# Performance work log

Hardware: AMD Instinct MI355X
Metric: run time of the kernel (lower is better)

Reference implementation:

```python
import jax, jax.numpy as jnp
import numpy as np

L = 8        # len_prog
E = 8        # experts per layer (uniform dsl_num)
D = 256      # embed_dim
B = 16384    # batch_size
H1, H2 = 64, 32  # MyMLP hidden dims


def setup_inputs() -> dict:
    key = jax.random.key(0)
    ks = jax.random.split(key, 8)
    s1 = 1.0 / np.sqrt(D)
    s2 = 1.0 / np.sqrt(H1)
    s3 = 1.0 / np.sqrt(H2)
    return {
        "src_embeddings": jax.random.normal(ks[0], (B, D), jnp.float32),
        "W1": jax.random.normal(ks[1], (L, E, H1, D), jnp.float32) * s1,
        "b1": jax.random.normal(ks[2], (L, E, H1), jnp.float32) * s1,
        "W2": jax.random.normal(ks[3], (L, E, H2, H1), jnp.float32) * s2,
        "b2": jax.random.normal(ks[4], (L, E, H2), jnp.float32) * s2,
        "W3": jax.random.normal(ks[5], (L, E, D, H2), jnp.float32) * s3,
        "b3": jax.random.normal(ks[6], (L, E, D), jnp.float32) * s3,
        "masks": jax.random.normal(ks[7], (L, B, E), jnp.float32) * 0.1,
    }


def reference(src_embeddings, W1, b1, W2, b2, W3, b3, masks):
    # Per layer: run E small expert MLPs on the same x, then combine with
    # softmax(mask) over the expert axis (torch path: masks=None -> softmax).
    def layer(x, params):
        w1, bb1, w2, bb2, w3, bb3, m = params
        h = jax.nn.relu(jnp.einsum('bd,ehd->beh', x, w1) + bb1)      # [B,E,H1]
        h = jax.nn.relu(jnp.einsum('beh,ekh->bek', h, w2) + bb2)     # [B,E,H2]
        out = jnp.einsum('bek,edk->bed', h, w3) + bb3                # [B,E,D]
        w = jax.nn.softmax(m, axis=-1)                               # [B,E]
        x_new = jnp.einsum('be,bed->bd', w, out)                     # [B,D]
        return x_new, None

    x, _ = jax.lax.scan(layer, src_embeddings, (W1, b1, W2, b2, W3, b3, masks))
    return x
```

## Files before the change

kernel.cpp:

```cpp
#include <hip/hip_runtime.h>
#include <hip/hip_bf16.h>

#define LNUM 8
#define ENUM 8
#define DDIM 256
#define BSZ  16384
#define H1N  64
#define H2N  32

#define BT   32
#define NTHR 256

#define PX   264
#define PH1  72
#define PH2  40
#define PSW  9

#define WS1_OFF 0
#define WS2_OFF 1048576
#define WS3_OFF 1179648

typedef float f32x4 __attribute__((ext_vector_type(4)));
typedef unsigned short u16x8 __attribute__((ext_vector_type(8)));
typedef unsigned short u16x4 __attribute__((ext_vector_type(4)));
typedef __bf16 bf16x8 __attribute__((ext_vector_type(8)));

#define Z4 ((f32x4){0.f, 0.f, 0.f, 0.f})

static __device__ __forceinline__ unsigned short f2bf(float f) {
    __bf16 h = (__bf16)f;
    return __builtin_bit_cast(unsigned short, h);
}

static __device__ __forceinline__ f32x4 mfma16(u16x8 a, u16x8 b, f32x4 c) {
    return __builtin_amdgcn_mfma_f32_16x16x32_bf16(
        __builtin_bit_cast(bf16x8, a), __builtin_bit_cast(bf16x8, b), c, 0, 0, 0);
}

static __device__ __forceinline__ void lbar() {
    asm volatile("s_waitcnt lgkmcnt(0)" ::: "memory");
    __builtin_amdgcn_s_barrier();
    asm volatile("" ::: "memory");
}

__global__ __launch_bounds__(256) void cvt_w_frag(
    const float* __restrict__ w1, const float* __restrict__ w2,
    const float* __restrict__ w3, unsigned short* __restrict__ ws)
{
    int gid = blockIdx.x * 256 + threadIdx.x;
    const float* src;
    unsigned short* dst;
    if (gid < 131072) {
        int s = gid >> 11, rem = gid & 2047;
        int n = rem >> 5, kc = rem & 31;
        int nt = n >> 4, r = n & 15, kt = kc >> 2, q = kc & 3;
        src = w1 + (size_t)gid * 8;
        dst = ws + WS1_OFF + (size_t)s * 16384 + nt * 4096 + kt * 512 + (q * 16 + r) * 8;
    } else if (gid < 147456) {
        int g = gid - 131072;
        int s = g >> 8, rem = g & 255;
        int n = rem >> 3, kc = rem & 7;
        int n2 = n >> 4, r = n & 15, kt = kc >> 2, q = kc & 3;
        src = w2 + (size_t)g * 8;
        dst = ws + WS2_OFF + (size_t)s * 2048 + n2 * 1024 + kt * 512 + (q * 16 + r) * 8;
    } else {
        int g = gid - 147456;
        int s = g >> 10, rem = g & 1023;
        int n = rem >> 2, q = rem & 3;
        int nt = n >> 4, r = n & 15;
        src = w3 + (size_t)g * 8;
        dst = ws + WS3_OFF + (size_t)s * 8192 + nt * 512 + (q * 16 + r) * 8;
    }
    float4 a = *(const float4*)src;
    float4 b = *(const float4*)(src + 4);
    u16x8 p;
    p[0] = f2bf(a.x); p[1] = f2bf(a.y); p[2] = f2bf(a.z); p[3] = f2bf(a.w);
    p[4] = f2bf(b.x); p[5] = f2bf(b.y); p[6] = f2bf(b.z); p[7] = f2bf(b.w);
    *(u16x8*)dst = p;
}

__global__ __launch_bounds__(NTHR, 2) void moe_fused(
    const float* __restrict__ src, const unsigned short* __restrict__ Wf,
    const float* __restrict__ b1, const float* __restrict__ b2,
    const float* __restrict__ b3, const float* __restrict__ masks,
    float* __restrict__ out)
{
    __shared__ __align__(16) unsigned short Xlds[BT * PX];
    __shared__ __align__(16) unsigned short H1T[2][BT * PH1];
    __shared__ __align__(16) unsigned short H2T[2][BT * PH2];
    __shared__ float SWlds[BT * PSW];

    const int tid  = threadIdx.x;
    const int lane = tid & 63;
    const int wn   = tid >> 6;
    const int rg   = wn & 1;
    const int fg   = wn >> 1;
    const int n15  = lane & 15;
    const int q    = lane >> 4;
    const int b0   = blockIdx.x * BT;

    const unsigned short* w1base = Wf + WS1_OFF + wn * 4096 + lane * 8;
    const unsigned short* w2base = Wf + WS2_OFF + fg * 1024 + lane * 8;
    const unsigned short* w3base = Wf + WS3_OFF + wn * 2048 + lane * 8;

    u16x8 xf[2][8];
    f32x4 ACC[2][4];

    auto stage_softmax = [&](int l) {
        if (tid < BT) {
            const float* mp = masks + ((size_t)l * BSZ + b0 + tid) * ENUM;
            float4 m0 = *(const float4*)mp;
            float4 m1 = *(const float4*)(mp + 4);
            float mv[8] = {m0.x, m0.y, m0.z, m0.w, m1.x, m1.y, m1.z, m1.w};
            float mx = mv[0];
            #pragma unroll
            for (int e = 1; e < 8; ++e) mx = fmaxf(mx, mv[e]);
            float s = 0.f;
            #pragma unroll
            for (int e = 0; e < 8; ++e) { mv[e] = expf(mv[e] - mx); s += mv[e]; }
            float inv = 1.f / s;
            #pragma unroll
            for (int e = 0; e < 8; ++e) SWlds[tid * PSW + e] = mv[e] * inv;
        }
    };

    auto acc_init = [&](int l) {
        const float* b3l = b3 + (size_t)l * ENUM * DDIM;
        #pragma unroll
        for (int mt = 0; mt < 2; ++mt)
            #pragma unroll
            for (int nt = 0; nt < 4; ++nt) ACC[mt][nt] = Z4;
        #pragma unroll 2
        for (int e2 = 0; e2 < ENUM; ++e2) {
            float swv[2][4];
            #pragma unroll
            for (int mt = 0; mt < 2; ++mt)
                #pragma unroll
                for (int rr = 0; rr < 4; ++rr)
                    swv[mt][rr] = SWlds[(mt*16 + q*4 + rr) * PSW + e2];
            #pragma unroll
            for (int nt = 0; nt < 4; ++nt) {
                float bv = b3l[e2 * DDIM + wn*64 + nt*16 + n15];
                #pragma unroll
                for (int mt = 0; mt < 2; ++mt)
                    #pragma unroll
                    for (int rr = 0; rr < 4; ++rr)
                        ACC[mt][nt][rr] += swv[mt][rr] * bv;
            }
        }
    };

    auto xf_read = [&]() {
        #pragma unroll
        for (int mt = 0; mt < 2; ++mt)
            #pragma unroll
            for (int kt = 0; kt < 8; ++kt)
                xf[mt][kt] = *(const u16x8*)
                    &Xlds[(mt*16 + n15) * PX + q*8 + kt*32];
    };
    auto x_write = [&]() {
        #pragma unroll
        for (int mt = 0; mt < 2; ++mt)
            #pragma unroll
            for (int nt = 0; nt < 4; ++nt)
                #pragma unroll
                for (int rr = 0; rr < 4; ++rr)
                    Xlds[(mt*16 + q*4 + rr) * PX + wn*64 + nt*16 + n15] =
                        f2bf(ACC[mt][nt][rr]);
    };

    #pragma unroll
    for (int i = 0; i < 4; ++i) {
        int o = (i * NTHR + tid) * 8;
        int r = o >> 8, c = o & 255;
        const float* p = src + (size_t)(b0 + r) * DDIM + c;
        float4 f0 = *(const float4*)(p);
        float4 f1 = *(const float4*)(p + 4);
        u16x8 pk;
        pk[0] = f2bf(f0.x); pk[1] = f2bf(f0.y); pk[2] = f2bf(f0.z); pk[3] = f2bf(f0.w);
        pk[4] = f2bf(f1.x); pk[5] = f2bf(f1.y); pk[6] = f2bf(f1.z); pk[7] = f2bf(f1.w);
        *(u16x8*)&Xlds[r * PX + c] = pk;
    }
    stage_softmax(0);
    __syncthreads();
    xf_read();
    acc_init(0);

    #pragma unroll 1
    for (int ss = 0; ss < LNUM * ENUM / 2; ++ss) {
        const int s0 = 2 * ss, s1 = s0 + 1;
        const int l  = s0 >> 3, e0 = s0 & 7, e1 = s1 & 7;

        u16x8 wfA[8], wfB[8], w2A[2], w2B[2];
        {
            const unsigned short* pA = w1base + (size_t)s0 * 16384;
            const unsigned short* pB = w1base + (size_t)s1 * 16384;
            #pragma unroll
            for (int kt = 0; kt < 8; ++kt) {
                wfA[kt] = *(const u16x8*)(pA + kt * 512);
                wfB[kt] = *(const u16x8*)(pB + kt * 512);
            }
            const unsigned short* q2A = w2base + (size_t)s0 * 2048;
            const unsigned short* q2B = w2base + (size_t)s1 * 2048;
            w2A[0] = *(const u16x8*)(q2A);  w2A[1] = *(const u16x8*)(q2A + 512);
            w2B[0] = *(const u16x8*)(q2B);  w2B[1] = *(const u16x8*)(q2B + 512);
        }
        const float4 bb1A = *(const float4*)(b1 + s0 * 64 + wn * 16 + q * 4);
        const float4 bb1B = *(const float4*)(b1 + s1 * 64 + wn * 16 + q * 4);
        const float4 bb2A = *(const float4*)(b2 + s0 * 32 + fg * 16 + q * 4);
        const float4 bb2B = *(const float4*)(b2 + s1 * 32 + fg * 16 + q * 4);

        f32x4 a1A[2] = {Z4, Z4}, a1B[2] = {Z4, Z4};
        #pragma unroll
        for (int kt = 0; kt < 8; ++kt) {
            a1A[0] = mfma16(wfA[kt], xf[0][kt], a1A[0]);
            a1A[1] = mfma16(wfA[kt], xf[1][kt], a1A[1]);
            a1B[0] = mfma16(wfB[kt], xf[0][kt], a1B[0]);
            a1B[1] = mfma16(wfB[kt], xf[1][kt], a1B[1]);
        }

        u16x8 w3A[4], w3B[4];
        {
            const unsigned short* p3A = w3base + (size_t)s0 * 8192;
            const unsigned short* p3B = w3base + (size_t)s1 * 8192;
            #pragma unroll
            for (int nt = 0; nt < 4; ++nt) {
                w3A[nt] = *(const u16x8*)(p3A + nt * 512);
                w3B[nt] = *(const u16x8*)(p3B + nt * 512);
            }
        }

        #pragma unroll
        for (int mt = 0; mt < 2; ++mt) {
            u16x4 pkA, pkB;
            #pragma unroll
            for (int rr = 0; rr < 4; ++rr) {
                pkA[rr] = f2bf(fmaxf(a1A[mt][rr] + bb1A[rr], 0.f));
                pkB[rr] = f2bf(fmaxf(a1B[mt][rr] + bb1B[rr], 0.f));
            }
            int row = mt*16 + n15;
            *(u16x4*)&H1T[0][row * PH1 + wn*16 + q*4] = pkA;
            *(u16x4*)&H1T[1][row * PH1 + wn*16 + q*4] = pkB;
        }
        lbar();

        f32x4 a2A = Z4, a2B = Z4;
        {
            int hrow = rg*16 + n15;
            u16x8 hA0 = *(const u16x8*)&H1T[0][hrow * PH1 + q*8];
            u16x8 hA1 = *(const u16x8*)&H1T[0][hrow * PH1 + q*8 + 32];
            u16x8 hB0 = *(const u16x8*)&H1T[1][hrow * PH1 + q*8];
            u16x8 hB1 = *(const u16x8*)&H1T[1][hrow * PH1 + q*8 + 32];
            a2A = mfma16(w2A[0], hA0, a2A);
            a2B = mfma16(w2B[0], hB0, a2B);
            a2A = mfma16(w2A[1], hA1, a2A);
            a2B = mfma16(w2B[1], hB1, a2B);
        }
        {
            int row = rg*16 + n15;
            float swA = SWlds[row * PSW + e0];
            float swB = SWlds[row * PSW + e1];
            u16x4 pkA, pkB;
            #pragma unroll
            for (int rr = 0; rr < 4; ++rr) {
                pkA[rr] = f2bf(fmaxf(a2A[rr] + bb2A[rr], 0.f) * swA);
                pkB[rr] = f2bf(fmaxf(a2B[rr] + bb2B[rr], 0.f) * swB);
            }
            *(u16x4*)&H2T[0][row * PH2 + fg*16 + q*4] = pkA;
            *(u16x4*)&H2T[1][row * PH2 + fg*16 + q*4] = pkB;
        }
        lbar();

        {
            u16x8 hA0 = *(const u16x8*)&H2T[0][(n15) * PH2 + q*8];
            u16x8 hA1 = *(const u16x8*)&H2T[0][(16 + n15) * PH2 + q*8];
            u16x8 hB0 = *(const u16x8*)&H2T[1][(n15) * PH2 + q*8];
            u16x8 hB1 = *(const u16x8*)&H2T[1][(16 + n15) * PH2 + q*8];
            #pragma unroll
            for (int nt = 0; nt < 4; ++nt) {
                ACC[0][nt] = mfma16(hA0, w3A[nt], ACC[0][nt]);
                ACC[1][nt] = mfma16(hA1, w3A[nt], ACC[1][nt]);
            }
            #pragma unroll
            for (int nt = 0; nt < 4; ++nt) {
                ACC[0][nt] = mfma16(hB0, w3B[nt], ACC[0][nt]);
                ACC[1][nt] = mfma16(hB1, w3B[nt], ACC[1][nt]);
            }
        }

        if (e1 == 7 && l < LNUM - 1) {
            x_write();
            lbar();
            xf_read();
            stage_softmax(l + 1);
            lbar();
            acc_init(l + 1);
        }
    }

    #pragma unroll
    for (int mt = 0; mt < 2; ++mt)
        #pragma unroll
        for (int nt = 0; nt < 4; ++nt)
            #pragma unroll
            for (int rr = 0; rr < 4; ++rr)
                out[(size_t)(b0 + mt*16 + q*4 + rr) * DDIM
                    + wn*64 + nt*16 + n15] = ACC[mt][nt][rr];
}

extern "C" void kernel_launch(void* const* d_in, const int* in_sizes, int n_in,
                              void* d_out, int out_size, void* d_ws, size_t ws_size,
                              hipStream_t stream) {
    const float* src   = (const float*)d_in[0];
    const float* W1    = (const float*)d_in[1];
    const float* b1    = (const float*)d_in[2];
    const float* W2    = (const float*)d_in[3];
    const float* b2    = (const float*)d_in[4];
    const float* W3    = (const float*)d_in[5];
    const float* b3    = (const float*)d_in[6];
    const float* masks = (const float*)d_in[7];
    float* out = (float*)d_out;
    unsigned short* ws = (unsigned short*)d_ws;

    hipLaunchKernelGGL(cvt_w_frag, dim3(832), dim3(256), 0, stream, W1, W2, W3, ws);
    hipLaunchKernelGGL(moe_fused, dim3(BSZ / BT), dim3(NTHR), 0, stream,
                       src, ws, b1, b2, b3, masks, out);
}
```

Before: 178.1 us.

## Software-pipeline the three expert GEMM stages across expert pairs with double-buffered LDS

Restructures the per-layer loop so that G1 of the next expert pair, G2 of the current pair and G3 of the previous pair run in the same barrier interval. H1T and H2T get double buffers indexed by parity, which cuts the number of barriers per expert pair. It also raises launch bounds to 4 waves-per-EU occupancy and adds s_setprio around the MFMA bursts. The cost is higher register pressure under the tighter occupancy target, with possible spilling, plus more LDS per block.

```diff
diff --git a/kernel.cpp b/kernel.cpp
--- a/kernel.cpp
+++ b/kernel.cpp
@@ -79,15 +79,15 @@
     *(u16x8*)dst = p;
 }
 
-__global__ __launch_bounds__(NTHR, 2) void moe_fused(
+__global__ __launch_bounds__(NTHR, 4) void moe_fused(
     const float* __restrict__ src, const unsigned short* __restrict__ Wf,
     const float* __restrict__ b1, const float* __restrict__ b2,
     const float* __restrict__ b3, const float* __restrict__ masks,
     float* __restrict__ out)
 {
     __shared__ __align__(16) unsigned short Xlds[BT * PX];
-    __shared__ __align__(16) unsigned short H1T[2][BT * PH1];
-    __shared__ __align__(16) unsigned short H2T[2][BT * PH2];
+    __shared__ __align__(16) unsigned short H1T[2][2][BT * PH1];
+    __shared__ __align__(16) unsigned short H2T[2][2][BT * PH2];
     __shared__ float SWlds[BT * PSW];
 
     const int tid  = threadIdx.x;
@@ -167,6 +167,109 @@
                 for (int rr = 0; rr < 4; ++rr)
                     Xlds[(mt*16 + q*4 + rr) * PX + wn*64 + nt*16 + n15] =
                         f2bf(ACC[mt][nt][rr]);
+    };
+
+    auto load_W1p = [&](int P, u16x8* A, u16x8* B) {
+        const unsigned short* pA = w1base + (size_t)(2*P) * 16384;
+        const unsigned short* pB = pA + 16384;
+        #pragma unroll
+        for (int kt = 0; kt < 8; ++kt) {
+            A[kt] = *(const u16x8*)(pA + kt * 512);
+            B[kt] = *(const u16x8*)(pB + kt * 512);
+        }
+    };
+    auto load_W2p = [&](int P, u16x8* A, u16x8* B) {
+        const unsigned short* qA = w2base + (size_t)(2*P) * 2048;
+        const unsigned short* qB = qA + 2048;
+        A[0] = *(const u16x8*)(qA);  A[1] = *(const u16x8*)(qA + 512);
+        B[0] = *(const u16x8*)(qB);  B[1] = *(const u16x8*)(qB + 512);
+    };
+    auto load_W3p = [&](int P, u16x8* A, u16x8* B) {
+        const unsigned short* pA = w3base + (size_t)(2*P) * 8192;
+        const unsigned short* pB = pA + 8192;
+        #pragma unroll
+        for (int nt = 0; nt < 4; ++nt) {
+            A[nt] = *(const u16x8*)(pA + nt * 512);
+            B[nt] = *(const u16x8*)(pB + nt * 512);
+        }
+    };
+
+    auto do_G1 = [&](int par, const u16x8* wfA, const u16x8* wfB,
+                     float4 bb1A, float4 bb1B) {
+        f32x4 a1A[2] = {Z4, Z4}, a1B[2] = {Z4, Z4};
+        __builtin_amdgcn_s_setprio(1);
+        #pragma unroll
+        for (int kt = 0; kt < 8; ++kt) {
+            a1A[0] = mfma16(wfA[kt], xf[0][kt], a1A[0]);
+            a1A[1] = mfma16(wfA[kt], xf[1][kt], a1A[1]);
+            a1B[0] = mfma16(wfB[kt], xf[0][kt], a1B[0]);
+            a1B[1] = mfma16(wfB[kt], xf[1][kt], a1B[1]);
+        }
+        __builtin_amdgcn_s_setprio(0);
+        #pragma unroll
+        for (int mt = 0; mt < 2; ++mt) {
+            u16x4 pkA, pkB;
+            #pragma unroll
+            for (int rr = 0; rr < 4; ++rr) {
+                pkA[rr] = f2bf(fmaxf(a1A[mt][rr] + bb1A[rr], 0.f));
+                pkB[rr] = f2bf(fmaxf(a1B[mt][rr] + bb1B[rr], 0.f));
+            }
+            int row = mt*16 + n15;
+            *(u16x4*)&H1T[par][0][row * PH1 + wn*16 + q*4] = pkA;
+            *(u16x4*)&H1T[par][1][row * PH1 + wn*16 + q*4] = pkB;
+        }
+    };
+
+    auto do_G2 = [&](int e0, int par, const u16x8* w2A, const u16x8* w2B,
+                     float4 bb2A, float4 bb2B) {
+        f32x4 a2A = Z4, a2B = Z4;
+        int hrow = rg*16 + n15;
+        u16x8 hA0 = *(const u16x8*)&H1T[par][0][hrow * PH1 + q*8];
+        u16x8 hA1 = *(const u16x8*)&H1T[par][0][hrow * PH1 + q*8 + 32];
+        u16x8 hB0 = *(const u16x8*)&H1T[par][1][hrow * PH1 + q*8];
+        u16x8 hB1 = *(const u16x8*)&H1T[par][1][hrow * PH1 + q*8 + 32];
+        a2A = mfma16(w2A[0], hA0, a2A);
+        a2B = mfma16(w2B[0], hB0, a2B);
+        a2A = mfma16(w2A[1], hA1, a2A);
+        a2B = mfma16(w2B[1], hB1, a2B);
+        float swA = SWlds[hrow * PSW + e0];
+        float swB = SWlds[hrow * PSW + e0 + 1];
+        u16x4 pkA, pkB;
+        #pragma unroll
+        for (int rr = 0; rr < 4; ++rr) {
+            pkA[rr] = f2bf(fmaxf(a2A[rr] + bb2A[rr], 0.f) * swA);
+            pkB[rr] = f2bf(fmaxf(a2B[rr] + bb2B[rr], 0.f) * swB);
+        }
+        *(u16x4*)&H2T[par][0][hrow * PH2 + fg*16 + q*4] = pkA;
+        *(u16x4*)&H2T[par][1][hrow * PH2 + fg*16 + q*4] = pkB;
+    };
+
+    auto do_G3 = [&](int par, const u16x8* w3A, const u16x8* w3B) {
+        u16x8 hA0 = *(const u16x8*)&H2T[par][0][(n15) * PH2 + q*8];
+        u16x8 hA1 = *(const u16x8*)&H2T[par][0][(16 + n15) * PH2 + q*8];
+        u16x8 hB0 = *(const u16x8*)&H2T[par][1][(n15) * PH2 + q*8];
+        u16x8 hB1 = *(const u16x8*)&H2T[par][1][(16 + n15) * PH2 + q*8];
+        __builtin_amdgcn_s_setprio(1);
+        #pragma unroll
+        for (int nt = 0; nt < 4; ++nt) {
+            ACC[0][nt] = mfma16(hA0, w3A[nt], ACC[0][nt]);
+            ACC[1][nt] = mfma16(hA1, w3A[nt], ACC[1][nt]);
+        }
+        #pragma unroll
+        for (int nt = 0; nt < 4; ++nt) {
+            ACC[0][nt] = mfma16(hB0, w3B[nt], ACC[0][nt]);
+            ACC[1][nt] = mfma16(hB1, w3B[nt], ACC[1][nt]);
+        }
+        __builtin_amdgcn_s_setprio(0);
+    };
+
+    auto ld_bb1 = [&](int P, float4& A, float4& B) {
+        A = *(const float4*)(b1 + (2*P) * 64 + wn * 16 + q * 4);
+        B = *(const float4*)(b1 + (2*P + 1) * 64 + wn * 16 + q * 4);
+    };
+    auto ld_bb2 = [&](int P, float4& A, float4& B) {
+        A = *(const float4*)(b2 + (2*P) * 32 + fg * 16 + q * 4);
+        B = *(const float4*)(b2 + (2*P + 1) * 32 + fg * 16 + q * 4);
     };
 
     #pragma unroll
@@ -187,108 +290,62 @@
     acc_init(0);
 
     #pragma unroll 1
-    for (int ss = 0; ss < LNUM * ENUM / 2; ++ss) {
-        const int s0 = 2 * ss, s1 = s0 + 1;
-        const int l  = s0 >> 3, e0 = s0 & 7, e1 = s1 & 7;
-
-        u16x8 wfA[8], wfB[8], w2A[2], w2B[2];
-        {
-            const unsigned short* pA = w1base + (size_t)s0 * 16384;
-            const unsigned short* pB = w1base + (size_t)s1 * 16384;
-            #pragma unroll
-            for (int kt = 0; kt < 8; ++kt) {
-                wfA[kt] = *(const u16x8*)(pA + kt * 512);
-                wfB[kt] = *(const u16x8*)(pB + kt * 512);
-            }
-            const unsigned short* q2A = w2base + (size_t)s0 * 2048;
-            const unsigned short* q2B = w2base + (size_t)s1 * 2048;
-            w2A[0] = *(const u16x8*)(q2A);  w2A[1] = *(const u16x8*)(q2A + 512);
-            w2B[0] = *(const u16x8*)(q2B);  w2B[1] = *(const u16x8*)(q2B + 512);
-        }
-        const float4 bb1A = *(const float4*)(b1 + s0 * 64 + wn * 16 + q * 4);
-        const float4 bb1B = *(const float4*)(b1 + s1 * 64 + wn * 16 + q * 4);
-        const float4 bb2A = *(const float4*)(b2 + s0 * 32 + fg * 16 + q * 4);
-        const float4 bb2B = *(const float4*)(b2 + s1 * 32 + fg * 16 + q * 4);
-
-        f32x4 a1A[2] = {Z4, Z4}, a1B[2] = {Z4, Z4};
-        #pragma unroll
-        for (int kt = 0; kt < 8; ++kt) {
-            a1A[0] = mfma16(wfA[kt], xf[0][kt], a1A[0]);
-            a1A[1] = mfma16(wfA[kt], xf[1][kt], a1A[1]);
-            a1B[0] = mfma16(wfB[kt], xf[0][kt], a1B[0]);
-            a1B[1] = mfma16(wfB[kt], xf[1][kt], a1B[1]);
-        }
-
-        u16x8 w3A[4], w3B[4];
-        {
-            const unsigned short* p3A = w3base + (size_t)s0 * 8192;
-            const unsigned short* p3B = w3base + (size_t)s1 * 8192;
-            #pragma unroll
-            for (int nt = 0; nt < 4; ++nt) {
-                w3A[nt] = *(const u16x8*)(p3A + nt * 512);
-                w3B[nt] = *(const u16x8*)(p3B + nt * 512);
-            }
-        }
-
-        #pragma unroll
-        for (int mt = 0; mt < 2; ++mt) {
-            u16x4 pkA, pkB;
-            #pragma unroll
-            for (int rr = 0; rr < 4; ++rr) {
-                pkA[rr] = f2bf(fmaxf(a1A[mt][rr] + bb1A[rr], 0.f));
-                pkB[rr] = f2bf(fmaxf(a1B[mt][rr] + bb1B[rr], 0.f));
-            }
-            int row = mt*16 + n15;
-            *(u16x4*)&H1T[0][row * PH1 + wn*16 + q*4] = pkA;
-            *(u16x4*)&H1T[1][row * PH1 + wn*16 + q*4] = pkB;
-        }
-        lbar();
-
-        f32x4 a2A = Z4, a2B = Z4;
-        {
-            int hrow = rg*16 + n15;
-            u16x8 hA0 = *(const u16x8*)&H1T[0][hrow * PH1 + q*8];
-            u16x8 hA1 = *(const u16x8*)&H1T[0][hrow * PH1 + q*8 + 32];
-            u16x8 hB0 = *(const u16x8*)&H1T[1][hrow * PH1 + q*8];
-            u16x8 hB1 = *(const u16x8*)&H1T[1][hrow * PH1 + q*8 + 32];
-            a2A = mfma16(w2A[0], hA0, a2A);
-            a2B = mfma16(w2B[0], hB0, a2B);
-            a2A = mfma16(w2A[1], hA1, a2A);
-            a2B = mfma16(w2B[1], hB1, a2B);
-        }
-        {
-            int row = rg*16 + n15;
-            float swA = SWlds[row * PSW + e0];
-            float swB = SWlds[row * PSW + e1];
-            u16x4 pkA, pkB;
-            #pragma unroll
-            for (int rr = 0; rr < 4; ++rr) {
-                pkA[rr] = f2bf(fmaxf(a2A[rr] + bb2A[rr], 0.f) * swA);
-                pkB[rr] = f2bf(fmaxf(a2B[rr] + bb2B[rr], 0.f) * swB);
-            }
-            *(u16x4*)&H2T[0][row * PH2 + fg*16 + q*4] = pkA;
-            *(u16x4*)&H2T[1][row * PH2 + fg*16 + q*4] = pkB;
-        }
-        lbar();
-
-        {
-            u16x8 hA0 = *(const u16x8*)&H2T[0][(n15) * PH2 + q*8];
-            u16x8 hA1 = *(const u16x8*)&H2T[0][(16 + n15) * PH2 + q*8];
-            u16x8 hB0 = *(const u16x8*)&H2T[1][(n15) * PH2 + q*8];
-            u16x8 hB1 = *(const u16x8*)&H2T[1][(16 + n15) * PH2 + q*8];
-            #pragma unroll
-            for (int nt = 0; nt < 4; ++nt) {
-                ACC[0][nt] = mfma16(hA0, w3A[nt], ACC[0][nt]);
-                ACC[1][nt] = mfma16(hA1, w3A[nt], ACC[1][nt]);
-            }
-            #pragma unroll
-            for (int nt = 0; nt < 4; ++nt) {
-                ACC[0][nt] = mfma16(hB0, w3B[nt], ACC[0][nt]);
-                ACC[1][nt] = mfma16(hB1, w3B[nt], ACC[1][nt]);
-            }
-        }
-
-        if (e1 == 7 && l < LNUM - 1) {
+    for (int l = 0; l < LNUM; ++l) {
+        const int P0 = 4 * l;
+
+        {
+            u16x8 wfA[8], wfB[8]; float4 bb1A, bb1B;
+            load_W1p(P0, wfA, wfB); ld_bb1(P0, bb1A, bb1B);
+            do_G1(0, wfA, wfB, bb1A, bb1B);
+            lbar();
+        }
+        {
+            u16x8 w2A[2], w2B[2], wfA[8], wfB[8];
+            float4 bb2A, bb2B, bb1A, bb1B;
+            load_W2p(P0, w2A, w2B); load_W1p(P0 + 1, wfA, wfB);
+            ld_bb2(P0, bb2A, bb2B); ld_bb1(P0 + 1, bb1A, bb1B);
+            do_G2(0, 0, w2A, w2B, bb2A, bb2B);
+            do_G1(1, wfA, wfB, bb1A, bb1B);
+            lbar();
+        }
+        {
+            u16x8 w2A[2], w2B[2], w3A[4], w3B[4], wfA[8], wfB[8];
+            float4 bb2A, bb2B, bb1A, bb1B;
+            load_W2p(P0 + 1, w2A, w2B); load_W3p(P0, w3A, w3B);
+            load_W1p(P0 + 2, wfA, wfB);
+            ld_bb2(P0 + 1, bb2A, bb2B); ld_bb1(P0 + 2, bb1A, bb1B);
+            do_G2(2, 1, w2A, w2B, bb2A, bb2B);
+            do_G3(0, w3A, w3B);
+            do_G1(0, wfA, wfB, bb1A, bb1B);
+            lbar();
+        }
+        {
+            u16x8 w2A[2], w2B[2], w3A[4], w3B[4], wfA[8], wfB[8];
+            float4 bb2A, bb2B, bb1A, bb1B;
+            load_W2p(P0 + 2, w2A, w2B); load_W3p(P0 + 1, w3A, w3B);
+            load_W1p(P0 + 3, wfA, wfB);
+            ld_bb2(P0 + 2, bb2A, bb2B); ld_bb1(P0 + 3, bb1A, bb1B);
+            do_G2(4, 0, w2A, w2B, bb2A, bb2B);
+            do_G3(1, w3A, w3B);
+            do_G1(1, wfA, wfB, bb1A, bb1B);
+            lbar();
+        }
+        {
+            u16x8 w2A[2], w2B[2], w3A[4], w3B[4];
+            float4 bb2A, bb2B;
+            load_W2p(P0 + 3, w2A, w2B); load_W3p(P0 + 2, w3A, w3B);
+            ld_bb2(P0 + 3, bb2A, bb2B);
+            do_G2(6, 1, w2A, w2B, bb2A, bb2B);
+            do_G3(0, w3A, w3B);
+            lbar();
+        }
+        {
+            u16x8 w3A[4], w3B[4];
+            load_W3p(P0 + 3, w3A, w3B);
+            do_G3(1, w3A, w3B);
+        }
+
+        if (l < LNUM - 1) {
             x_write();
             lbar();
             xf_read();
```

Result: slower. 243.1 us (+36.5%).

## Assign whole experts per wave for stages 1-2 to cut block barriers

Applied to the files above, without the earlier changes.

Instead of all four waves cooperating on each expert pair, which needs two block barriers per pair, each wave now computes the full first and second MLP layers for two experts privately. It uses a per-wave H1 buffer and writes all eight H2 tiles to LDS. A single barrier per layer precedes the cooperative third-layer accumulation over all experts. This removes most barriers, but increases per-wave register pressure, LDS footprint, and the serial first-layer work per wave.

```diff
diff --git a/kernel.cpp b/kernel.cpp
--- a/kernel.cpp
+++ b/kernel.cpp
@@ -86,22 +86,18 @@
     float* __restrict__ out)
 {
     __shared__ __align__(16) unsigned short Xlds[BT * PX];
-    __shared__ __align__(16) unsigned short H1T[2][BT * PH1];
-    __shared__ __align__(16) unsigned short H2T[2][BT * PH2];
+    __shared__ __align__(16) unsigned short H1W[4][BT * PH1];
+    __shared__ __align__(16) unsigned short H2T[8][BT * PH2];
     __shared__ float SWlds[BT * PSW];
 
     const int tid  = threadIdx.x;
     const int lane = tid & 63;
-    const int wn   = tid >> 6;
-    const int rg   = wn & 1;
-    const int fg   = wn >> 1;
+    const int wv   = tid >> 6;
     const int n15  = lane & 15;
     const int q    = lane >> 4;
     const int b0   = blockIdx.x * BT;
 
-    const unsigned short* w1base = Wf + WS1_OFF + wn * 4096 + lane * 8;
-    const unsigned short* w2base = Wf + WS2_OFF + fg * 1024 + lane * 8;
-    const unsigned short* w3base = Wf + WS3_OFF + wn * 2048 + lane * 8;
+    const unsigned short* w3base = Wf + WS3_OFF + wv * 2048 + lane * 8;
 
     u16x8 xf[2][8];
     f32x4 ACC[2][4];
@@ -140,7 +136,7 @@
                     swv[mt][rr] = SWlds[(mt*16 + q*4 + rr) * PSW + e2];
             #pragma unroll
             for (int nt = 0; nt < 4; ++nt) {
-                float bv = b3l[e2 * DDIM + wn*64 + nt*16 + n15];
+                float bv = b3l[e2 * DDIM + wv*64 + nt*16 + n15];
                 #pragma unroll
                 for (int mt = 0; mt < 2; ++mt)
                     #pragma unroll
@@ -165,7 +161,7 @@
             for (int nt = 0; nt < 4; ++nt)
                 #pragma unroll
                 for (int rr = 0; rr < 4; ++rr)
-                    Xlds[(mt*16 + q*4 + rr) * PX + wn*64 + nt*16 + n15] =
+                    Xlds[(mt*16 + q*4 + rr) * PX + wv*64 + nt*16 + n15] =
                         f2bf(ACC[mt][nt][rr]);
     };
 
@@ -184,117 +180,111 @@
     stage_softmax(0);
     __syncthreads();
     xf_read();
-    acc_init(0);
 
     #pragma unroll 1
-    for (int ss = 0; ss < LNUM * ENUM / 2; ++ss) {
-        const int s0 = 2 * ss, s1 = s0 + 1;
-        const int l  = s0 >> 3, e0 = s0 & 7, e1 = s1 & 7;
-
-        u16x8 wfA[8], wfB[8], w2A[2], w2B[2];
-        {
-            const unsigned short* pA = w1base + (size_t)s0 * 16384;
-            const unsigned short* pB = w1base + (size_t)s1 * 16384;
-            #pragma unroll
-            for (int kt = 0; kt < 8; ++kt) {
-                wfA[kt] = *(const u16x8*)(pA + kt * 512);
-                wfB[kt] = *(const u16x8*)(pB + kt * 512);
+    for (int l = 0; l < LNUM; ++l) {
+        const int sbase = l * ENUM;
+
+        #pragma unroll
+        for (int pe = 0; pe < 2; ++pe) {
+            const int e = wv + pe * 4;
+            const int s = sbase + e;
+
+            #pragma unroll
+            for (int ft = 0; ft < 4; ++ft) {
+                u16x8 w1f[8];
+                const unsigned short* p1 =
+                    Wf + WS1_OFF + (size_t)s * 16384 + ft * 4096 + lane * 8;
+                #pragma unroll
+                for (int kt = 0; kt < 8; ++kt)
+                    w1f[kt] = *(const u16x8*)(p1 + kt * 512);
+                f32x4 a1[2] = {Z4, Z4};
+                #pragma unroll
+                for (int kt = 0; kt < 8; ++kt) {
+                    a1[0] = mfma16(w1f[kt], xf[0][kt], a1[0]);
+                    a1[1] = mfma16(w1f[kt], xf[1][kt], a1[1]);
+                }
+                const float4 bb1 = *(const float4*)(b1 + s * 64 + ft * 16 + q * 4);
+                #pragma unroll
+                for (int mt = 0; mt < 2; ++mt) {
+                    u16x4 pk;
+                    #pragma unroll
+                    for (int rr = 0; rr < 4; ++rr)
+                        pk[rr] = f2bf(fmaxf(a1[mt][rr] + bb1[rr], 0.f));
+                    *(u16x4*)&H1W[wv][(mt*16 + n15) * PH1 + ft*16 + q*4] = pk;
+                }
             }
-            const unsigned short* q2A = w2base + (size_t)s0 * 2048;
-            const unsigned short* q2B = w2base + (size_t)s1 * 2048;
-            w2A[0] = *(const u16x8*)(q2A);  w2A[1] = *(const u16x8*)(q2A + 512);
-            w2B[0] = *(const u16x8*)(q2B);  w2B[1] = *(const u16x8*)(q2B + 512);
-        }
-        const float4 bb1A = *(const float4*)(b1 + s0 * 64 + wn * 16 + q * 4);
-        const float4 bb1B = *(const float4*)(b1 + s1 * 64 + wn * 16 + q * 4);
-        const float4 bb2A = *(const float4*)(b2 + s0 * 32 + fg * 16 + q * 4);
-        const float4 bb2B = *(const float4*)(b2 + s1 * 32 + fg * 16 + q * 4);
-
-        f32x4 a1A[2] = {Z4, Z4}, a1B[2] = {Z4, Z4};
-        #pragma unroll
-        for (int kt = 0; kt < 8; ++kt) {
-            a1A[0] = mfma16(wfA[kt], xf[0][kt], a1A[0]);
-            a1A[1] = mfma16(wfA[kt], xf[1][kt], a1A[1]);
-            a1B[0] = mfma16(wfB[kt], xf[0][kt], a1B[0]);
-            a1B[1] = mfma16(wfB[kt], xf[1][kt], a1B[1]);
-        }
-
-        u16x8 w3A[4], w3B[4];
-        {
-            const unsigned short* p3A = w3base + (size_t)s0 * 8192;
-            const unsigned short* p3B = w3base + (size_t)s1 * 8192;
+
+            {
+                u16x8 w2f[2][2];
+                const unsigned short* p2 =
+                    Wf + WS2_OFF + (size_t)s * 2048 + lane * 8;
+                #pragma unroll
+                for (int f2 = 0; f2 < 2; ++f2)
+                    #pragma unroll
+                    for (int kt = 0; kt < 2; ++kt)
+                        w2f[f2][kt] = *(const u16x8*)(p2 + f2*1024 + kt*512);
+                u16x8 h1f[2][2];
+                #pragma unroll
+                for (int mt = 0; mt < 2; ++mt)
+                    #pragma unroll
+                    for (int kt = 0; kt < 2; ++kt)
+                        h1f[mt][kt] = *(const u16x8*)
+                            &H1W[wv][(mt*16 + n15) * PH1 + q*8 + kt*32];
+                f32x4 a2[2][2] = {{Z4, Z4}, {Z4, Z4}};
+                #pragma unroll
+                for (int f2 = 0; f2 < 2; ++f2)
+                    #pragma unroll
+                    for (int mt = 0; mt < 2; ++mt)
+                        #pragma unroll
+                        for (int kt = 0; kt < 2; ++kt)
+                            a2[f2][mt] = mfma16(w2f[f2][kt], h1f[mt][kt], a2[f2][mt]);
+                float swv[2];
+                #pragma unroll
+                for (int mt = 0; mt < 2; ++mt)
+                    swv[mt] = SWlds[(mt*16 + n15) * PSW + e];
+                #pragma unroll
+                for (int f2 = 0; f2 < 2; ++f2) {
+                    const float4 bb2 = *(const float4*)(b2 + s * 32 + f2 * 16 + q * 4);
+                    #pragma unroll
+                    for (int mt = 0; mt < 2; ++mt) {
+                        u16x4 pk;
+                        #pragma unroll
+                        for (int rr = 0; rr < 4; ++rr)
+                            pk[rr] = f2bf(fmaxf(a2[f2][mt][rr] + bb2[rr], 0.f) * swv[mt]);
+                        *(u16x4*)&H2T[e][(mt*16 + n15) * PH2 + f2*16 + q*4] = pk;
+                    }
+                }
+            }
+        }
+
+        lbar();
+
+        acc_init(l);
+
+        #pragma unroll
+        for (int e = 0; e < ENUM; ++e) {
+            const int s = sbase + e;
+            u16x8 w3f[4];
+            const unsigned short* p3 = w3base + (size_t)s * 8192;
+            #pragma unroll
+            for (int nt = 0; nt < 4; ++nt)
+                w3f[nt] = *(const u16x8*)(p3 + nt * 512);
+            u16x8 h0 = *(const u16x8*)&H2T[e][(n15) * PH2 + q*8];
+            u16x8 h1v = *(const u16x8*)&H2T[e][(16 + n15) * PH2 + q*8];
             #pragma unroll
             for (int nt = 0; nt < 4; ++nt) {
-                w3A[nt] = *(const u16x8*)(p3A + nt * 512);
-                w3B[nt] = *(const u16x8*)(p3B + nt * 512);
+                ACC[0][nt] = mfma16(h0,  w3f[nt], ACC[0][nt]);
+                ACC[1][nt] = mfma16(h1v, w3f[nt], ACC[1][nt]);
             }
         }
 
-        #pragma unroll
-        for (int mt = 0; mt < 2; ++mt) {
-            u16x4 pkA, pkB;
-            #pragma unroll
-            for (int rr = 0; rr < 4; ++rr) {
-                pkA[rr] = f2bf(fmaxf(a1A[mt][rr] + bb1A[rr], 0.f));
-                pkB[rr] = f2bf(fmaxf(a1B[mt][rr] + bb1B[rr], 0.f));
-            }
-            int row = mt*16 + n15;
-            *(u16x4*)&H1T[0][row * PH1 + wn*16 + q*4] = pkA;
-            *(u16x4*)&H1T[1][row * PH1 + wn*16 + q*4] = pkB;
-        }
-        lbar();
-
-        f32x4 a2A = Z4, a2B = Z4;
-        {
-            int hrow = rg*16 + n15;
-            u16x8 hA0 = *(const u16x8*)&H1T[0][hrow * PH1 + q*8];
-            u16x8 hA1 = *(const u16x8*)&H1T[0][hrow * PH1 + q*8 + 32];
-            u16x8 hB0 = *(const u16x8*)&H1T[1][hrow * PH1 + q*8];
-            u16x8 hB1 = *(const u16x8*)&H1T[1][hrow * PH1 + q*8 + 32];
-            a2A = mfma16(w2A[0], hA0, a2A);
-            a2B = mfma16(w2B[0], hB0, a2B);
-            a2A = mfma16(w2A[1], hA1, a2A);
-            a2B = mfma16(w2B[1], hB1, a2B);
-        }
-        {
-            int row = rg*16 + n15;
-            float swA = SWlds[row * PSW + e0];
-            float swB = SWlds[row * PSW + e1];
-            u16x4 pkA, pkB;
-            #pragma unroll
-            for (int rr = 0; rr < 4; ++rr) {
-                pkA[rr] = f2bf(fmaxf(a2A[rr] + bb2A[rr], 0.f) * swA);
-                pkB[rr] = f2bf(fmaxf(a2B[rr] + bb2B[rr], 0.f) * swB);
-            }
-            *(u16x4*)&H2T[0][row * PH2 + fg*16 + q*4] = pkA;
-            *(u16x4*)&H2T[1][row * PH2 + fg*16 + q*4] = pkB;
-        }
-        lbar();
-
-        {
-            u16x8 hA0 = *(const u16x8*)&H2T[0][(n15) * PH2 + q*8];
-            u16x8 hA1 = *(const u16x8*)&H2T[0][(16 + n15) * PH2 + q*8];
-            u16x8 hB0 = *(const u16x8*)&H2T[1][(n15) * PH2 + q*8];
-            u16x8 hB1 = *(const u16x8*)&H2T[1][(16 + n15) * PH2 + q*8];
-            #pragma unroll
-            for (int nt = 0; nt < 4; ++nt) {
-                ACC[0][nt] = mfma16(hA0, w3A[nt], ACC[0][nt]);
-                ACC[1][nt] = mfma16(hA1, w3A[nt], ACC[1][nt]);
-            }
-            #pragma unroll
-            for (int nt = 0; nt < 4; ++nt) {
-                ACC[0][nt] = mfma16(hB0, w3B[nt], ACC[0][nt]);
-                ACC[1][nt] = mfma16(hB1, w3B[nt], ACC[1][nt]);
-            }
-        }
-
-        if (e1 == 7 && l < LNUM - 1) {
+        if (l < LNUM - 1) {
             x_write();
             lbar();
             xf_read();
             stage_softmax(l + 1);
             lbar();
-            acc_init(l + 1);
         }
     }
 
@@ -305,7 +295,7 @@
             #pragma unroll
             for (int rr = 0; rr < 4; ++rr)
                 out[(size_t)(b0 + mt*16 + q*4 + rr) * DDIM
-                    + wn*64 + nt*16 + n15] = ACC[mt][nt][rr];
+                    + wv*64 + nt*16 + n15] = ACC[mt][nt][rr];
 }
 
 extern "C" void kernel_launch(void* const* d_in, const int* in_sizes, int n_in,
```

New measurement: 175.5 us. No clear change (-1.5%).
